# Kernel tuning notes

Measured on AMD Instinct MI355X. Metric: run time of the kernel, lower is better.

## Reference

```python
import jax, jax.numpy as jnp
import numpy as np


def setup_inputs() -> dict:
    key = jax.random.key(0)
    k1, k2, k3, k4 = jax.random.split(key, 4)
    B, S, D, F = 16, 4096, 1024, 1024
    x = jax.random.normal(k1, (B, S, D), dtype=jnp.float32)
    # Keras 'normal' initializer ~ N(0, 0.05); scale similarly for realism
    W_key = jax.random.normal(k2, (D, F), dtype=jnp.float32) * 0.05
    W_query = jax.random.normal(k3, (D, F), dtype=jnp.float32) * 0.05
    W_value = jax.random.normal(k4, (D, F), dtype=jnp.float32) * 0.05
    return {"x": x, "W_key": W_key, "W_query": W_query, "W_value": W_value}


def reference(x, W_key, W_query, W_value):
    # x: [B,S,D]; W_*: [D,F]
    keys = jnp.tanh(jnp.einsum("bsd,df->bsf", x, W_key))
    query = jnp.tanh(jnp.einsum("bsd,df->bsf", x, W_query))
    value = jnp.tanh(jnp.einsum("bsd,df->bsf", x, W_value))
    # diag(Q K^T) == per-token dot product, computed directly in O(S*F)
    attn_scores = jnp.einsum("bsf,bsf->bs", query, keys)  # [B,S]
    attn_softmax = jax.nn.softmax(attn_scores, axis=-1)[..., None]  # [B,S,1]
    # value^T @ softmax -> [B,F,1]
    weighted_input = jnp.einsum("bsf,bso->bfo", value, attn_softmax)
    return weighted_input, attn_softmax
```

## Files before the change

kernel.cpp:

```cpp
#include <hip/hip_runtime.h>
#include <hip/hip_bf16.h>
#include <math.h>
#include <stdint.h>

typedef _Float16 f16;
typedef _Float16 half8 __attribute__((ext_vector_type(8)));
typedef float f32x4 __attribute__((ext_vector_type(4)));

#define B_ 16
#define S_ 4096
#define D_ 1024
#define F_ 1024
#define TOK (B_*S_)
#define TB3 128
#define FB3 64
#define NFB3 16
#define NT3 32
#define NSV 4
#define CSV (S_/NSV)

__device__ __forceinline__ void gload_lds16(const void* g, void* l) {
    __builtin_amdgcn_global_load_lds(
        (__attribute__((address_space(1))) const unsigned int*)(unsigned long long)(uintptr_t)g,
        (__attribute__((address_space(3))) unsigned int*)(unsigned int)(uintptr_t)l,
        16, 0, 0);
}

__device__ __forceinline__ void fma2(float2& a, float s, const float2& wv) {
    a.x += s * wv.x; a.y += s * wv.y;
}

__global__ void cvt_x(const float* __restrict__ x, f16* __restrict__ xh) {
    size_t i = ((size_t)blockIdx.x * 256 + threadIdx.x) * 8;
    float4 a = *(const float4*)(x + i);
    float4 b = *(const float4*)(x + i + 4);
    half8 h = {(f16)a.x,(f16)a.y,(f16)a.z,(f16)a.w,
               (f16)b.x,(f16)b.y,(f16)b.z,(f16)b.w};
    *(half8*)(xh + i) = h;
}

__global__ void cvt_w2(const float* __restrict__ Wk, const float* __restrict__ Wq,
                       f16* __restrict__ wtf) {
    const int gw   = blockIdx.x * 4 + (threadIdx.x >> 6);
    const int lane = threadIdx.x & 63;
    const int nblk = gw & 3, kt = (gw >> 2) & 31, fb = (gw >> 7) & 15, mat = gw >> 11;
    const float* W = mat ? Wq : Wk;
    const int f  = fb * 64 + nblk * 16 + (lane & 15);
    const int d0 = kt * 32 + (lane >> 4) * 8;
    half8 h;
#pragma unroll
    for (int e = 0; e < 8; ++e) h[e] = (f16)W[(size_t)(d0 + e) * F_ + f];
    *(half8*)(wtf + (size_t)gw * 512 + lane * 8) = h;
}

__launch_bounds__(256, 4)
__global__ void score_gemm(const f16* __restrict__ xh, const f16* __restrict__ wtf,
                           float* __restrict__ part) {
    __shared__ __align__(16) f16 Xs[4][TB3 * 32];
    __shared__ float sred[2][TB3];

    const int hid  = blockIdx.x;
    const int orig = (hid & 7) * 1024 + (hid >> 3);
    const int fb   = orig & 15;
    const int tok0 = (orig >> 4) * TB3;

    const int t = threadIdx.x, lane = t & 63, w = t >> 6;
    const int wr = (w >> 1) * 64;
    const int wc = (w & 1) * 32;

    const int rx0 = t >> 2,         qx0 = (t & 3) ^ ((rx0 >> 1) & 3);
    const int rx1 = (t + 256) >> 2, qx1 = (t & 3) ^ ((rx1 >> 1) & 3);
    const f16* srcX0 = xh + (size_t)(tok0 + rx0) * D_ + qx0 * 8;
    const f16* srcX1 = xh + (size_t)(tok0 + rx1) * D_ + qx1 * 8;
    const int wbase = w * 1024;

    int offA[4];
#pragma unroll
    for (int m = 0; m < 4; ++m) {
        int row = wr + m * 16 + (lane & 15);
        int q   = (lane >> 4) ^ ((row >> 1) & 3);
        offA[m] = row * 32 + q * 8;
    }

    const f16* bK = wtf + (((size_t)fb * NT3 * 4) + 2 * (w & 1)) * 512 + lane * 8;
    const f16* bQ = bK + (size_t)NFB3 * NT3 * 4 * 512;

#define STAGE_X(sl, kof) do {                                         \
        gload_lds16(srcX0 + (kof), (char*)Xs[sl] + wbase);            \
        gload_lds16(srcX1 + (kof), (char*)Xs[sl] + 4096 + wbase);     \
    } while (0)

    f32x4 accK[4][2] = {};
    f32x4 accQ[4][2] = {};
    half8 wKf[2][2], wQf[2][2];

    STAGE_X(0, 0);
    STAGE_X(1, 32);
    STAGE_X(2, 64);
#pragma unroll
    for (int n = 0; n < 2; ++n) {
        wKf[0][n] = *(const half8*)(bK + n * 512);
        wQf[0][n] = *(const half8*)(bQ + n * 512);
    }
    asm volatile("s_waitcnt vmcnt(8)" ::: "memory");
    __builtin_amdgcn_s_barrier();

#pragma unroll
    for (int kt = 0; kt < NT3; ++kt) {
        const int cur = kt & 3, par = kt & 1, nx = par ^ 1;
        if (kt < NT3 - 1) {
#pragma unroll
            for (int n = 0; n < 2; ++n) {
                wKf[nx][n] = *(const half8*)(bK + ((size_t)(kt + 1) * 4 + n) * 512);
                wQf[nx][n] = *(const half8*)(bQ + ((size_t)(kt + 1) * 4 + n) * 512);
            }
        }
        if (kt < NT3 - 3) STAGE_X((kt + 3) & 3, (kt + 3) * 32);

        half8 aF[4];
#pragma unroll
        for (int m = 0; m < 4; ++m) aF[m] = *(const half8*)(Xs[cur] + offA[m]);
#pragma unroll
        for (int n = 0; n < 2; ++n)
#pragma unroll
            for (int m = 0; m < 4; ++m) {
                accK[m][n] = __builtin_amdgcn_mfma_f32_16x16x32_f16(aF[m], wKf[par][n], accK[m][n], 0, 0, 0);
                accQ[m][n] = __builtin_amdgcn_mfma_f32_16x16x32_f16(aF[m], wQf[par][n], accQ[m][n], 0, 0, 0);
            }
        if (kt < NT3 - 1) __builtin_amdgcn_s_barrier();
    }
#undef STAGE_X

#pragma unroll
    for (int m = 0; m < 4; ++m) {
        float s[4] = {0.f, 0.f, 0.f, 0.f};
#pragma unroll
        for (int n = 0; n < 2; ++n)
#pragma unroll
            for (int j = 0; j < 4; ++j)
                s[j] += tanhf(accQ[m][n][j]) * tanhf(accK[m][n][j]);
#pragma unroll
        for (int j = 0; j < 4; ++j) {
            s[j] += __shfl_xor(s[j], 1);
            s[j] += __shfl_xor(s[j], 2);
            s[j] += __shfl_xor(s[j], 4);
            s[j] += __shfl_xor(s[j], 8);
        }
        if ((lane & 15) == 0) {
            int g = lane >> 4;
#pragma unroll
            for (int j = 0; j < 4; ++j)
                sred[w & 1][wr + m * 16 + g * 4 + j] = s[j];
        }
    }
    __syncthreads();
    if (t < TB3)
        part[(size_t)fb * TOK + tok0 + t] = sred[0][t] + sred[1][t];
}

__global__ void softmax_k(const float* __restrict__ part, float* __restrict__ out) {
    __shared__ float sc[S_];
    __shared__ float red[256];
    const int b = blockIdx.x, t = threadIdx.x;
    float lmax = -1e30f;
    for (int i = t; i < S_; i += 256) {
        float s = 0.f;
#pragma unroll
        for (int fb = 0; fb < NFB3; ++fb) s += part[(size_t)fb * TOK + b * S_ + i];
        sc[i] = s;
        lmax = fmaxf(lmax, s);
    }
    red[t] = lmax; __syncthreads();
    for (int o = 128; o > 0; o >>= 1) { if (t < o) red[t] = fmaxf(red[t], red[t + o]); __syncthreads(); }
    const float mx = red[0]; __syncthreads();
    float lsum = 0.f;
    for (int i = t; i < S_; i += 256) { float e = expf(sc[i] - mx); sc[i] = e; lsum += e; }
    red[t] = lsum; __syncthreads();
    for (int o = 128; o > 0; o >>= 1) { if (t < o) red[t] += red[t + o]; __syncthreads(); }
    const float inv = 1.0f / red[0];
    for (int i = t; i < S_; i += 256)
        out[(size_t)B_ * F_ + (size_t)b * S_ + i] = sc[i] * inv;
}

__launch_bounds__(512)
__global__ void value_k5(const float* __restrict__ x, const float* __restrict__ Wv,
                         const float* __restrict__ p_in, float* __restrict__ vpart) {
    __shared__ __align__(16) float xs[8][D_];
    __shared__ float ps[CSV];
    __shared__ int   idxs[CSV];
    __shared__ int   wsum[8];
    __shared__ int   rbase_s;
    const int b = blockIdx.x, c = blockIdx.y;
    const int t = threadIdx.x, lane = t & 63, w = t >> 6;
    const int s0 = c * CSV;

    if (t == 0) rbase_s = 0;
    __syncthreads();
#pragma unroll 1
    for (int r = 0; r < 2; ++r) {
        int i = r * 512 + t;
        float p = p_in[(size_t)b * S_ + s0 + i];
        bool flag = p > 1e-7f;
        unsigned long long mask = __ballot(flag);
        if (lane == 0) wsum[w] = __popcll(mask);
        __syncthreads();
        int base = rbase_s;
#pragma unroll
        for (int k = 0; k < 8; ++k) if (k < w) base += wsum[k];
        if (flag) {
            int pos = base + __popcll(mask & ((1ull << lane) - 1ull));
            idxs[pos] = s0 + i;
            ps[pos] = p;
        }
        __syncthreads();
        if (t == 0) {
            int sum = 0;
#pragma unroll
            for (int k = 0; k < 8; ++k) sum += wsum[k];
            rbase_s += sum;
        }
        __syncthreads();
    }
    const int cnt = rbase_s;

    float2 acc = {0.f, 0.f};
    for (int g = 0; g < cnt; g += 8) {
        __syncthreads();
        const int ng = cnt - g;
#pragma unroll
        for (int r = 0; r < 8; ++r) {
            float2 v = {0.f, 0.f};
            if (r < ng)
                v = ((const float2*)(x + ((size_t)b * S_ + idxs[g + r]) * D_))[t];
            ((float2*)xs[r])[t] = v;
        }
        __syncthreads();
        if (ng >= 5) {
            float2 a[8] = {};
#pragma unroll 2
            for (int dq = 0; dq < D_ / 4; ++dq) {
                const float* wrp = Wv + (size_t)dq * 4 * F_ + 2 * t;
                float2 wv0 = *(const float2*)(wrp         );
                float2 wv1 = *(const float2*)(wrp + F_    );
                float2 wv2 = *(const float2*)(wrp + 2 * F_);
                float2 wv3 = *(const float2*)(wrp + 3 * F_);
#pragma unroll
                for (int r = 0; r < 8; ++r) {
                    float4 xr = ((const float4*)xs[r])[dq];
                    fma2(a[r], xr.x, wv0); fma2(a[r], xr.y, wv1);
                    fma2(a[r], xr.z, wv2); fma2(a[r], xr.w, wv3);
                }
            }
#pragma unroll
            for (int r = 0; r < 8; ++r)
                if (g + r < cnt) {
                    float pw = ps[g + r];
                    acc.x += pw * tanhf(a[r].x);
                    acc.y += pw * tanhf(a[r].y);
                }
        } else {
            float2 a[4] = {};
#pragma unroll 2
            for (int dq = 0; dq < D_ / 4; ++dq) {
                const float* wrp = Wv + (size_t)dq * 4 * F_ + 2 * t;
                float2 wv0 = *(const float2*)(wrp         );
                float2 wv1 = *(const float2*)(wrp + F_    );
                float2 wv2 = *(const float2*)(wrp + 2 * F_);
                float2 wv3 = *(const float2*)(wrp + 3 * F_);
#pragma unroll
                for (int r = 0; r < 4; ++r) {
                    float4 xr = ((const float4*)xs[r])[dq];
                    fma2(a[r], xr.x, wv0); fma2(a[r], xr.y, wv1);
                    fma2(a[r], xr.z, wv2); fma2(a[r], xr.w, wv3);
                }
            }
#pragma unroll
            for (int r = 0; r < 4; ++r)
                if (g + r < cnt) {
                    float pw = ps[g + r];
                    acc.x += pw * tanhf(a[r].x);
                    acc.y += pw * tanhf(a[r].y);
                }
        }
    }
    ((float2*)(vpart + ((size_t)c * B_ + b) * F_))[t] = acc;
}

__global__ void value_red(const float* __restrict__ vpart, float* __restrict__ out) {
    int i = blockIdx.x * 256 + threadIdx.x;
    float s = 0.f;
#pragma unroll
    for (int c = 0; c < NSV; ++c) s += vpart[(size_t)c * B_ * F_ + i];
    out[i] = s;
}

extern "C" void kernel_launch(void* const* d_in, const int* in_sizes, int n_in,
                              void* d_out, int out_size, void* d_ws, size_t ws_size,
                              hipStream_t stream) {
    const float* x  = (const float*)d_in[0];
    const float* Wk = (const float*)d_in[1];
    const float* Wq = (const float*)d_in[2];
    const float* Wv = (const float*)d_in[3];
    float* out = (float*)d_out;
    char* ws = (char*)d_ws;

    f16*   xh   = (f16*)ws;
    f16*   wtf  = (f16*)(ws + (size_t)TOK * D_ * 2);
    float* part = (float*)(ws + (size_t)TOK * D_ * 2 + 2 * (size_t)D_ * F_ * 2);

    cvt_x<<<TOK * D_ / 8 / 256, 256, 0, stream>>>(x, xh);
    cvt_w2<<<1024, 256, 0, stream>>>(Wk, Wq, wtf);
    score_gemm<<<NFB3 * (TOK / TB3), 256, 0, stream>>>(xh, wtf, part);
    softmax_k<<<B_, 256, 0, stream>>>(part, out);
    float* vpart = part;
    const float* p_in = out + (size_t)B_ * F_;
    value_k5<<<dim3(B_, NSV), 512, 0, stream>>>(x, Wv, p_in, vpart);
    value_red<<<B_ * F_ / 256, 256, 0, stream>>>(vpart, out);
}
```

Measured before the change: 553.0 us.

## Retile score GEMM to 256x256 tiles with LDS-staged weights and ping-pong MFMA

Restructures the fused K/Q score GEMM from 128-token by 64-feature tiles, with weights read straight into registers, to 256-token by 256-column tiles (K and Q interleaved), staged in LDS for both operands, with 8 waves per block. The main loop splits into two half-steps with barriers, setprio and sched_barrier to overlap async global-to-LDS loads with MFMA bursts. Weights are re-laid out row-major per column block to suit the new staging, and the number of score partials drops from 16 to 8. The larger tile raises arithmetic intensity and reuse of x, at the cost of more LDS (128KB), fewer resident blocks and a more delicate vmcnt/barrier schedule.

```diff
diff --git a/kernel.cpp b/kernel.cpp
--- a/kernel.cpp
+++ b/kernel.cpp
@@ -12,10 +12,8 @@
 #define D_ 1024
 #define F_ 1024
 #define TOK (B_*S_)
-#define TB3 128
-#define FB3 64
-#define NFB3 16
-#define NT3 32
+#define NBN 8
+#define NKT 32
 #define NSV 4
 #define CSV (S_/NSV)
 
@@ -39,106 +37,109 @@
     *(half8*)(xh + i) = h;
 }
 
-__global__ void cvt_w2(const float* __restrict__ Wk, const float* __restrict__ Wq,
-                       f16* __restrict__ wtf) {
-    const int gw   = blockIdx.x * 4 + (threadIdx.x >> 6);
-    const int lane = threadIdx.x & 63;
-    const int nblk = gw & 3, kt = (gw >> 2) & 31, fb = (gw >> 7) & 15, mat = gw >> 11;
-    const float* W = mat ? Wq : Wk;
-    const int f  = fb * 64 + nblk * 16 + (lane & 15);
-    const int d0 = kt * 32 + (lane >> 4) * 8;
+__global__ void cvt_w3(const float* __restrict__ Wk, const float* __restrict__ Wq,
+                       f16* __restrict__ wt2) {
+    const int u = blockIdx.x * 256 + threadIdx.x;
+    const int c = u >> 7, dc = u & 127;
+    const int cc = c & 255, bn = c >> 8;
+    const float* W = ((cc >> 4) & 1) ? Wq : Wk;
+    const int f  = bn * 128 + (cc >> 5) * 16 + (cc & 15);
+    const int d0 = dc * 8;
     half8 h;
 #pragma unroll
     for (int e = 0; e < 8; ++e) h[e] = (f16)W[(size_t)(d0 + e) * F_ + f];
-    *(half8*)(wtf + (size_t)gw * 512 + lane * 8) = h;
-}
-
-__launch_bounds__(256, 4)
-__global__ void score_gemm(const f16* __restrict__ xh, const f16* __restrict__ wtf,
+    *(half8*)(wt2 + (size_t)c * D_ + d0) = h;
+}
+
+__launch_bounds__(512, 2)
+__global__ void score_gemm(const f16* __restrict__ xh, const f16* __restrict__ wt2,
                            float* __restrict__ part) {
-    __shared__ __align__(16) f16 Xs[4][TB3 * 32];
-    __shared__ float sred[2][TB3];
+    __shared__ __align__(16) f16 AB[2][4][256 * 32];
+    __shared__ float sred[4][256];
 
     const int hid  = blockIdx.x;
-    const int orig = (hid & 7) * 1024 + (hid >> 3);
-    const int fb   = orig & 15;
-    const int tok0 = (orig >> 4) * TB3;
+    const int orig = (hid & 7) * 256 + (hid >> 3);
+    const int bn   = orig & 7;
+    const int tok0 = (orig >> 3) * 256;
 
     const int t = threadIdx.x, lane = t & 63, w = t >> 6;
-    const int wr = (w >> 1) * 64;
-    const int wc = (w & 1) * 32;
-
-    const int rx0 = t >> 2,         qx0 = (t & 3) ^ ((rx0 >> 1) & 3);
-    const int rx1 = (t + 256) >> 2, qx1 = (t & 3) ^ ((rx1 >> 1) & 3);
-    const f16* srcX0 = xh + (size_t)(tok0 + rx0) * D_ + qx0 * 8;
-    const f16* srcX1 = xh + (size_t)(tok0 + rx1) * D_ + qx1 * 8;
-    const int wbase = w * 1024;
-
-    int offA[4];
-#pragma unroll
-    for (int m = 0; m < 4; ++m) {
-        int row = wr + m * 16 + (lane & 15);
-        int q   = (lane >> 4) ^ ((row >> 1) & 3);
-        offA[m] = row * 32 + q * 8;
-    }
-
-    const f16* bK = wtf + (((size_t)fb * NT3 * 4) + 2 * (w & 1)) * 512 + lane * 8;
-    const f16* bQ = bK + (size_t)NFB3 * NT3 * 4 * 512;
-
-#define STAGE_X(sl, kof) do {                                         \
-        gload_lds16(srcX0 + (kof), (char*)Xs[sl] + wbase);            \
-        gload_lds16(srcX1 + (kof), (char*)Xs[sl] + 4096 + wbase);     \
+    const int wr = w >> 2;
+    const int wc = w & 3;
+
+    const int srow = t >> 2;
+    const int qsw  = (t & 3) ^ ((t >> 3) & 3);
+    const f16* srcA = xh  + (size_t)(tok0 + srow) * D_ + qsw * 8;
+    const f16* srcB = wt2 + (size_t)(bn * 256 + srow) * D_ + qsw * 8;
+    const int wu = w * 1024;
+
+    const int kq   = ((lane >> 4) ^ ((lane >> 1) & 3)) * 16;
+    const int arow = (wr * 128 + (lane & 15)) * 64 + kq;
+    const int brow = (wc * 64  + (lane & 15)) * 64 + kq;
+
+#define STAGE(mat, kt, j) do {                                                   \
+        const f16* s_ = (mat) ? srcB : srcA;                                     \
+        gload_lds16(s_ + (size_t)(j) * 131072 + (kt) * 32,                       \
+                    (char*)AB + (mat) * 65536 + ((kt) & 3) * 16384 +             \
+                    (j) * 8192 + wu);                                            \
     } while (0)
 
-    f32x4 accK[4][2] = {};
-    f32x4 accQ[4][2] = {};
-    half8 wKf[2][2], wQf[2][2];
-
-    STAGE_X(0, 0);
-    STAGE_X(1, 32);
-    STAGE_X(2, 64);
-#pragma unroll
-    for (int n = 0; n < 2; ++n) {
-        wKf[0][n] = *(const half8*)(bK + n * 512);
-        wQf[0][n] = *(const half8*)(bQ + n * 512);
-    }
-    asm volatile("s_waitcnt vmcnt(8)" ::: "memory");
+    f32x4 acc[8][4] = {};
+
+    STAGE(0, 0, 0); STAGE(1, 0, 0); STAGE(0, 0, 1); STAGE(1, 0, 1);
+    STAGE(0, 1, 0); STAGE(1, 1, 0); STAGE(0, 1, 1); STAGE(1, 1, 1);
+    asm volatile("s_waitcnt vmcnt(4)" ::: "memory");
     __builtin_amdgcn_s_barrier();
 
-#pragma unroll
-    for (int kt = 0; kt < NT3; ++kt) {
-        const int cur = kt & 3, par = kt & 1, nx = par ^ 1;
-        if (kt < NT3 - 1) {
-#pragma unroll
-            for (int n = 0; n < 2; ++n) {
-                wKf[nx][n] = *(const half8*)(bK + ((size_t)(kt + 1) * 4 + n) * 512);
-                wQf[nx][n] = *(const half8*)(bQ + ((size_t)(kt + 1) * 4 + n) * 512);
-            }
-        }
-        if (kt < NT3 - 3) STAGE_X((kt + 3) & 3, (kt + 3) * 32);
-
-        half8 aF[4];
-#pragma unroll
-        for (int m = 0; m < 4; ++m) aF[m] = *(const half8*)(Xs[cur] + offA[m]);
-#pragma unroll
-        for (int n = 0; n < 2; ++n)
-#pragma unroll
-            for (int m = 0; m < 4; ++m) {
-                accK[m][n] = __builtin_amdgcn_mfma_f32_16x16x32_f16(aF[m], wKf[par][n], accK[m][n], 0, 0, 0);
-                accQ[m][n] = __builtin_amdgcn_mfma_f32_16x16x32_f16(aF[m], wQf[par][n], accQ[m][n], 0, 0, 0);
-            }
-        if (kt < NT3 - 1) __builtin_amdgcn_s_barrier();
-    }
-#undef STAGE_X
-
-#pragma unroll
-    for (int m = 0; m < 4; ++m) {
-        float s[4] = {0.f, 0.f, 0.f, 0.f};
-#pragma unroll
-        for (int n = 0; n < 2; ++n)
-#pragma unroll
-            for (int j = 0; j < 4; ++j)
-                s[j] += tanhf(accQ[m][n][j]) * tanhf(accK[m][n][j]);
+#pragma unroll 1
+    for (int kt = 0; kt < NKT; ++kt) {
+        const int sl = kt & 3;
+        const char* Ab = (const char*)AB + sl * 16384;
+        const char* Bb = (const char*)AB + 65536 + sl * 16384;
+        half8 aF[4], bF[4];
+
+#pragma unroll
+        for (int m = 0; m < 4; ++m) aF[m] = *(const half8*)(Ab + arow + m * 1024);
+#pragma unroll
+        for (int n = 0; n < 4; ++n) bF[n] = *(const half8*)(Bb + brow + n * 1024);
+        if (kt < NKT - 2) { STAGE(0, kt + 2, 0); STAGE(1, kt + 2, 0); }
+        __builtin_amdgcn_s_barrier();
+        asm volatile("s_waitcnt lgkmcnt(0)" ::: "memory");
+        __builtin_amdgcn_sched_barrier(0);
+        __builtin_amdgcn_s_setprio(1);
+#pragma unroll
+        for (int n = 0; n < 4; ++n)
+#pragma unroll
+            for (int m = 0; m < 4; ++m)
+                acc[m][n] = __builtin_amdgcn_mfma_f32_16x16x32_f16(aF[m], bF[n], acc[m][n], 0, 0, 0);
+        __builtin_amdgcn_s_setprio(0);
+        __builtin_amdgcn_s_barrier();
+
+#pragma unroll
+        for (int m = 0; m < 4; ++m) aF[m] = *(const half8*)(Ab + arow + (m + 4) * 1024);
+        if (kt < NKT - 2) { STAGE(0, kt + 2, 1); STAGE(1, kt + 2, 1); }
+        if (kt < NKT - 2)      { asm volatile("s_waitcnt vmcnt(4)" ::: "memory"); }
+        else if (kt == NKT - 2){ asm volatile("s_waitcnt vmcnt(0)" ::: "memory"); }
+        __builtin_amdgcn_s_barrier();
+        asm volatile("s_waitcnt lgkmcnt(0)" ::: "memory");
+        __builtin_amdgcn_sched_barrier(0);
+        __builtin_amdgcn_s_setprio(1);
+#pragma unroll
+        for (int n = 0; n < 4; ++n)
+#pragma unroll
+            for (int m = 0; m < 4; ++m)
+                acc[m + 4][n] = __builtin_amdgcn_mfma_f32_16x16x32_f16(aF[m], bF[n], acc[m + 4][n], 0, 0, 0);
+        __builtin_amdgcn_s_setprio(0);
+        if (kt < NKT - 1) __builtin_amdgcn_s_barrier();
+    }
+#undef STAGE
+
+#pragma unroll
+    for (int m = 0; m < 8; ++m) {
+        float s[4];
+#pragma unroll
+        for (int j = 0; j < 4; ++j)
+            s[j] = tanhf(acc[m][1][j]) * tanhf(acc[m][0][j])
+                 + tanhf(acc[m][3][j]) * tanhf(acc[m][2][j]);
 #pragma unroll
         for (int j = 0; j < 4; ++j) {
             s[j] += __shfl_xor(s[j], 1);
@@ -150,12 +151,13 @@
             int g = lane >> 4;
 #pragma unroll
             for (int j = 0; j < 4; ++j)
-                sred[w & 1][wr + m * 16 + g * 4 + j] = s[j];
+                sred[wc][wr * 128 + m * 16 + g * 4 + j] = s[j];
         }
     }
     __syncthreads();
-    if (t < TB3)
-        part[(size_t)fb * TOK + tok0 + t] = sred[0][t] + sred[1][t];
+    if (t < 256)
+        part[(size_t)bn * TOK + tok0 + t] =
+            sred[0][t] + sred[1][t] + sred[2][t] + sred[3][t];
 }
 
 __global__ void softmax_k(const float* __restrict__ part, float* __restrict__ out) {
@@ -166,7 +168,7 @@
     for (int i = t; i < S_; i += 256) {
         float s = 0.f;
 #pragma unroll
-        for (int fb = 0; fb < NFB3; ++fb) s += part[(size_t)fb * TOK + b * S_ + i];
+        for (int bn = 0; bn < NBN; ++bn) s += part[(size_t)bn * TOK + b * S_ + i];
         sc[i] = s;
         lmax = fmaxf(lmax, s);
     }
@@ -305,12 +307,12 @@
     char* ws = (char*)d_ws;
 
     f16*   xh   = (f16*)ws;
-    f16*   wtf  = (f16*)(ws + (size_t)TOK * D_ * 2);
+    f16*   wt2  = (f16*)(ws + (size_t)TOK * D_ * 2);
     float* part = (float*)(ws + (size_t)TOK * D_ * 2 + 2 * (size_t)D_ * F_ * 2);
 
     cvt_x<<<TOK * D_ / 8 / 256, 256, 0, stream>>>(x, xh);
-    cvt_w2<<<1024, 256, 0, stream>>>(Wk, Wq, wtf);
-    score_gemm<<<NFB3 * (TOK / TB3), 256, 0, stream>>>(xh, wtf, part);
+    cvt_w3<<<1024, 256, 0, stream>>>(Wk, Wq, wt2);
+    score_gemm<<<NBN * (TOK / 256), 512, 0, stream>>>(xh, wt2, part);
     softmax_k<<<B_, 256, 0, stream>>>(part, out);
     float* vpart = part;
     const float* p_in = out + (size_t)B_ * F_;
```

Result: slower. 598.9 us (+8.3%).
